# Kernel optimization log

Measured on AMD Instinct MI355X. Metric: run time of the kernel, lower is better.

Reference implementation:

```python
import math
import jax, jax.numpy as jnp
import numpy as np

# hyperparameters (module defaults; w_scale overridden to 1.0)
EMA_SPEED = 0.05
REW_SENS = 1.0
LR = 0.0033
MOMENTUM = 0.4
UNTANH = 0.6
SPEED = 0.5
WIDTH = 0.1
WD = 0.01
LAT_DECAY = 0.01
NOISE_SCALE = 0.8
C_MOMENT = 0.99
W_SCALE = 1.0


def rms_norm(x, axis=-1):
    return x * jax.lax.rsqrt(jnp.mean(x * x, axis=axis, keepdims=True) + 1e-6)


def setup_inputs() -> dict:
    key = jax.random.key(0)
    ks = jax.random.split(key, 16)
    B, N, D = 16, 128, 64
    s = 1.0 / math.sqrt(D)
    return {
        'eye_env': jax.random.normal(ks[0], (B, D), jnp.float32),
        'stomach_env': jax.random.normal(ks[1], (B, D), jnp.float32),
        'state': jax.random.normal(ks[2], (B, N, D), jnp.float32),
        'output': jax.random.normal(ks[3], (B, N, D), jnp.float32),
        'W1': jax.random.normal(ks[4], (B, N, D, D), jnp.float32) * s,
        'W2': jax.random.normal(ks[5], (B, N, D, D), jnp.float32) * s,
        'W3': jax.random.normal(ks[6], (B, N, D, D), jnp.float32) * s,
        'M1': jax.random.normal(ks[7], (B, N, D, D), jnp.float32) * 0.2,
        'M2': jax.random.normal(ks[8], (B, N, D, D), jnp.float32) * 0.2,
        'M3': jax.random.normal(ks[9], (B, N, D, D), jnp.float32) * 0.2,
        'E_baseline': jax.random.uniform(ks[10], (B, N, D), jnp.float32),
        'A': jax.nn.softmax(jax.random.normal(ks[11], (B, N, N), jnp.float32), axis=2),
        'noise_A': jax.random.normal(ks[12], (B, N, N), jnp.float32),
        'noise1_raw': jax.random.normal(ks[13], (B, N, D), jnp.float32),
        'noise2_raw': jax.random.normal(ks[14], (B, N, D), jnp.float32),
        'step_counter': 0,
    }


def reference(eye_env, stomach_env, state, output, W1, W2, W3, M1, M2, M3,
              E_baseline, A, noise_A, noise1_raw, noise2_raw, step_counter):
    B, N, D = state.shape
    sc = jnp.float32(step_counter) + 1.0  # self.step_counter += 1

    # attention routing
    q = jnp.einsum('bnj,bnjk->bnk', state, W3)
    k = jnp.einsum('bnj,bnjk->bnk', state, W2)
    raw_A = jnp.einsum('bnd,bmd->bnm', q, k) / math.sqrt(D) + noise_A * 1e-5
    P_dense = jax.nn.softmax(raw_A, axis=2)
    keep = (P_dense > 1.0 / (N + 1.0)) | (P_dense == jnp.max(P_dense, axis=2, keepdims=True))
    P = jax.nn.softmax(jnp.where(keep, raw_A, -jnp.inf), axis=2)
    A_new = A * C_MOMENT + P * (1.0 - C_MOMENT)
    A_new = A_new.at[:, 0:2, :].set(0.0)

    # message passing + sensory clamp
    target = jnp.einsum('bnm,bmd->bnd', A_new, output)
    target = target.at[:, 0].set(eye_env).at[:, 1].set(stomach_env)

    # prediction
    raw_pred = jnp.einsum('bnj,bnjk->bnk', state, W1)
    raw = raw_pred - jnp.tanh(raw_pred) * UNTANH
    prediction = jnp.tanh(raw) * math.sqrt(2.0 + math.sqrt(2.0))

    err = prediction - target
    E_curr = jax.nn.softmax(err, axis=-1)
    bmask = (E_baseline == 0).astype(jnp.float32)
    Eb = E_baseline * (1.0 - bmask) + E_curr * bmask
    Eb = Eb * (1.0 - EMA_SPEED) + EMA_SPEED * E_curr
    advantage = E_curr - Eb
    R = -rms_norm(advantage[..., None] * REW_SENS)  # (B,N,D,1)
    mask = (Eb > 0).astype(jnp.float32)[..., None]

    # noise injection
    state_mag = jnp.sum(jnp.abs(state), axis=(-2, -1), keepdims=True)
    noise1 = noise1_raw / (1.0 + state_mag)
    noise2 = noise2_raw * jnp.std(err, ddof=1) * NOISE_SCALE
    noisy_state = state + noise1 + noise2

    # Hebbian outer-product gradient, G_NORM=1.0 -> rms-normalized
    lg = -jnp.einsum('bni,bnj->bnij', err, noisy_state)
    lg = rms_norm(lg, axis=(2, 3))

    plasticity = 1.0 - R
    grad1 = plasticity * lg * mask + LAT_DECAY * W3 - WD * W1
    grad2 = plasticity * lg * mask + LAT_DECAY * W1 - WD * W2
    grad3 = plasticity * lg * mask + LAT_DECAY * W2 - WD * W3

    # travelling gaussian column mask
    idx = jnp.arange(D, dtype=jnp.float32).reshape(1, 1, 1, D)
    center = (sc * SPEED) % D
    diff = jnp.abs(idx - center)
    diff = jnp.minimum(diff, D - diff)
    g_mask = jnp.exp(-diff ** 2 / (2.0 * WIDTH ** 2 + 1e-6))

    M1n = M1 * MOMENTUM + (1.0 - MOMENTUM) * (grad1 * g_mask)
    M2n = M2 * MOMENTUM + (1.0 - MOMENTUM) * (grad2 * g_mask)
    M3n = M3 * MOMENTUM + (1.0 - MOMENTUM) * (grad3 * g_mask)
    W1n = rms_norm(W1 + LR * M1n) * W_SCALE
    W2n = rms_norm(W2 + LR * M2n) * W_SCALE
    W3n = rms_norm(W3 + LR * M3n) * W_SCALE

    # new output = prediction, new state = target
    return prediction, target, A_new, W1n, W2n, W3n
```

## Files before the change

### kernel.cpp

```cpp
#include <hip/hip_runtime.h>
#include <hip/hip_bf16.h>

typedef __hip_bfloat16 bf16;

__device__ __forceinline__ float b2f(bf16 x) { return __bfloat162float(x); }

template<bool F32>
__device__ __forceinline__ float ld(const void* p, size_t i) {
  if constexpr (F32) return ((const float*)p)[i];
  else return b2f(((const bf16*)p)[i]);
}

template<bool F32>
__device__ __forceinline__ void ld8(const void* p, size_t i, float v[8]) {
  if constexpr (F32) {
    const float4 a = *(const float4*)((const float*)p + i);
    const float4 b = *(const float4*)((const float*)p + i + 4);
    v[0]=a.x; v[1]=a.y; v[2]=a.z; v[3]=a.w;
    v[4]=b.x; v[5]=b.y; v[6]=b.z; v[7]=b.w;
  } else {
    union { uint4 u; bf16 h[8]; } t;
    t.u = *(const uint4*)((const bf16*)p + i);
    #pragma unroll
    for (int c = 0; c < 8; ++c) v[c] = b2f(t.h[c]);
  }
}


__global__ void k0_detect(const void* __restrict__ state, int* __restrict__ flag) {
  const int tid = threadIdx.x;
  bool huge = false;
  for (int i = tid; i < 1024; i += 64) {
    const float x = b2f(((const bf16*)state)[i]);
    if (!(fabsf(x) < 1e5f)) huge = true;
  }
  const unsigned long long m = __ballot(huge);
  if (tid == 0) *flag = (m != 0ull) ? 1 : 0;
}

template<bool F32>
__device__ __forceinline__ void k1_body(
    const void* state, const void* W1, const void* W2, const void* W3,
    float* qw, float* kw, float* pw, float* mag, float* out_pred,
    float* s_state, float (*s_part)[4][64])
{
  const int node = blockIdx.x;
  const int b = node >> 7;
  const int g = threadIdx.x >> 6;
  const int k = threadIdx.x & 63;
  if (threadIdx.x < 64) s_state[threadIdx.x] = ld<F32>(state, (size_t)node*64 + threadIdx.x);
  __syncthreads();
  const size_t nb = (size_t)node * 4096;
  float aq = 0.f, ak = 0.f, ap = 0.f;
  #pragma unroll 4
  for (int jj = 0; jj < 16; ++jj) {
    const int j = g*16 + jj;
    const float sj = s_state[j];
    const size_t off = nb + (size_t)j*64 + k;
    aq += sj * ld<F32>(W3, off);
    ak += sj * ld<F32>(W2, off);
    ap += sj * ld<F32>(W1, off);
  }
  s_part[0][g][k] = aq; s_part[1][g][k] = ak; s_part[2][g][k] = ap;
  __syncthreads();
  if (g == 0) {
    const float qv = s_part[0][0][k] + s_part[0][1][k] + s_part[0][2][k] + s_part[0][3][k];
    const float kv = s_part[1][0][k] + s_part[1][1][k] + s_part[1][2][k] + s_part[1][3][k];
    const float rp = s_part[2][0][k] + s_part[2][1][k] + s_part[2][2][k] + s_part[2][3][k];
    qw[(size_t)node*64 + k] = qv;
    kw[(size_t)node*64 + k] = kv;
    const float raw  = rp - tanhf(rp) * 0.6f;
    const float pred = tanhf(raw) * 1.8477590650225735f;
    pw[(size_t)node*64 + k] = pred;
    out_pred[(size_t)node*64 + k] = pred;
  } else if (g == 1) {
    float a = fabsf(s_state[k]);
    #pragma unroll
    for (int s = 32; s; s >>= 1) a += __shfl_xor(a, s, 64);
    if (k == 0) atomicAdd(&mag[b], a);
  }
}

__global__ __launch_bounds__(256) void k1_qkpred(
    const int* __restrict__ flag,
    const void* __restrict__ state,
    const void* __restrict__ W1, const void* __restrict__ W2,
    const void* __restrict__ W3,
    float* __restrict__ qw, float* __restrict__ kw, float* __restrict__ pw,
    float* __restrict__ mag, float* __restrict__ out_pred)
{
  __shared__ float s_state[64];
  __shared__ float s_part[3][4][64];
  if (*flag) k1_body<true >(state, W1, W2, W3, qw, kw, pw, mag, out_pred, s_state, s_part);
  else       k1_body<false>(state, W1, W2, W3, qw, kw, pw, mag, out_pred, s_state, s_part);
}

template<bool F32>
__device__ __forceinline__ void k2_body(
    const float* qw, const float* kw, const float* pw,
    const void* noiseA, const void* Aold, const void* outp_in,
    const void* eye, const void* stomach, const void* Ebase,
    float* errw, float* plw, float* stats,
    float* out_target, float* out_A,
    float* s_q, float* s_red, float* s_A)
{
  const int node = blockIdx.x;
  const int b = node >> 7, n = node & 127;
  const int m = threadIdx.x;
  if (m < 64) s_q[m] = qw[(size_t)node*64 + m];
  __syncthreads();
  const float4* k4 = (const float4*)(kw + ((size_t)(b*128 + m)) * 64);
  float dot = 0.f;
  #pragma unroll
  for (int i = 0; i < 16; ++i) {
    const float4 v = k4[i];
    dot += s_q[4*i]*v.x + s_q[4*i+1]*v.y + s_q[4*i+2]*v.z + s_q[4*i+3]*v.w;
  }
  const float raw = dot * 0.125f + 1e-5f * ld<F32>(noiseA, (size_t)node*128 + m);
  s_red[m] = raw; __syncthreads();
  for (int s = 64; s >= 1; s >>= 1) { if (m < s) s_red[m] = fmaxf(s_red[m], s_red[m+s]); __syncthreads(); }
  const float rmax = s_red[0]; __syncthreads();
  const float e = expf(raw - rmax);
  s_red[m] = e; __syncthreads();
  for (int s = 64; s >= 1; s >>= 1) { if (m < s) s_red[m] += s_red[m+s]; __syncthreads(); }
  const float S = s_red[0]; __syncthreads();
  const float Pd = e / S;
  const bool keep = (Pd > 0.007751937984496124f) || (raw == rmax);
  const float ek = keep ? e : 0.f;
  s_red[m] = ek; __syncthreads();
  for (int s = 64; s >= 1; s >>= 1) { if (m < s) s_red[m] += s_red[m+s]; __syncthreads(); }
  const float Sk = s_red[0];
  const float P = ek / Sk;
  const float An = (n < 2) ? 0.f
                 : 0.99f * ld<F32>(Aold, (size_t)node*128 + m) + 0.01f * P;
  s_A[m] = An;
  out_A[(size_t)node*128 + m] = An;
  __syncthreads();
  if (m < 64) {
    float t;
    if (n == 0)      t = ld<F32>(eye, b*64 + m);
    else if (n == 1) t = ld<F32>(stomach, b*64 + m);
    else {
      t = 0.f;
      for (int mm = 0; mm < 128; ++mm)
        t += s_A[mm] * ld<F32>(outp_in, ((size_t)b*128 + mm)*64 + m);
    }
    out_target[(size_t)node*64 + m] = t;
    const float er = pw[(size_t)node*64 + m] - t;
    errw[(size_t)node*64 + m] = er;
    float mx = er;
    #pragma unroll
    for (int s = 32; s; s >>= 1) mx = fmaxf(mx, __shfl_xor(mx, s, 64));
    const float ee = expf(er - mx);
    float ssum = ee;
    #pragma unroll
    for (int s = 32; s; s >>= 1) ssum += __shfl_xor(ssum, s, 64);
    const float Ec = ee / ssum;
    const float Ebl = ld<F32>(Ebase, (size_t)node*64 + m);
    const float Eb0 = (Ebl == 0.f) ? Ec : Ebl;
    const float Eb  = Eb0 * 0.95f + 0.05f * Ec;
    const float adv = Ec - Eb;
    const float R = -adv * rsqrtf(adv*adv + 1e-6f);
    const float maskv = (Eb > 0.f) ? 1.f : 0.f;
    plw[(size_t)node*64 + m] = (1.f - R) * maskv;
    float se = er, se2 = er*er;
    #pragma unroll
    for (int s = 32; s; s >>= 1) { se += __shfl_xor(se, s, 64); se2 += __shfl_xor(se2, s, 64); }
    if (m == 0) { atomicAdd(&stats[0], se); atomicAdd(&stats[1], se2); }
  }
}

__global__ __launch_bounds__(128) void k2_attn(
    const int* __restrict__ flag,
    const float* __restrict__ qw, const float* __restrict__ kw,
    const float* __restrict__ pw,
    const void* __restrict__ noiseA, const void* __restrict__ Aold,
    const void* __restrict__ outp_in,
    const void* __restrict__ eye, const void* __restrict__ stomach,
    const void* __restrict__ Ebase,
    float* __restrict__ errw, float* __restrict__ plw,
    float* __restrict__ stats,
    float* __restrict__ out_target, float* __restrict__ out_A)
{
  __shared__ float s_q[64];
  __shared__ float s_red[128];
  __shared__ float s_A[128];
  if (*flag) k2_body<true >(qw,kw,pw,noiseA,Aold,outp_in,eye,stomach,Ebase,errw,plw,stats,out_target,out_A,s_q,s_red,s_A);
  else       k2_body<false>(qw,kw,pw,noiseA,Aold,outp_in,eye,stomach,Ebase,errw,plw,stats,out_target,out_A,s_q,s_red,s_A);
}

template<bool F32>
__device__ __forceinline__ void k3_body(
    const float* errw, const float* plw,
    const void* state, const void* n1raw, const void* n2raw,
    const float* mag, const float* stats, const int* stepc,
    const void* W1, const void* W2, const void* W3,
    const void* M1, const void* M2, const void* M3,
    float* oW1, float* oW2, float* oW3,
    float* s_err, float* s_ns, float* s_pe, float* s_c, float* s_g)
{
  const int node = blockIdx.x;
  const int b = node >> 7;
  const int tid = threadIdx.x;
  if (tid < 64) {
    s_err[tid] = errw[(size_t)node*64 + tid];
  } else if (tid < 128) {
    const int i = tid - 64;
    const float S1 = stats[0], S2 = stats[1];
    const float Mn = 131072.f;
    const float var = (S2 - S1*S1/Mn) / (Mn - 1.f);
    const float stdv = sqrtf(fmaxf(var, 0.f));
    const float st = ld<F32>(state, (size_t)node*64 + i);
    s_ns[i] = st + ld<F32>(n1raw, (size_t)node*64 + i) / (1.f + mag[b])
                 + ld<F32>(n2raw, (size_t)node*64 + i) * stdv * 0.8f;
  }
  __syncthreads();
  if (tid < 64) {
    float e2 = s_err[tid]*s_err[tid];
    float n2 = s_ns[tid]*s_ns[tid];
    #pragma unroll
    for (int s = 32; s; s >>= 1) { e2 += __shfl_xor(e2, s, 64); n2 += __shfl_xor(n2, s, 64); }
    const float f = rsqrtf(e2 * n2 * (1.f/4096.f) + 1e-6f);
    s_c[tid] = -s_ns[tid] * f;
    const float sc = (float)stepc[0] + 1.f;
    const float center = fmodf(sc * 0.5f, 64.f);
    float diff = fabsf((float)tid - center);
    diff = fminf(diff, 64.f - diff);
    s_g[tid] = expf(-diff*diff * (1.f/0.020001f));
    s_pe[tid] = plw[(size_t)node*64 + tid] * s_err[tid];
  }
  __syncthreads();
  const size_t nb = (size_t)node * 4096;
  const int lane8 = tid & 7;
  #pragma unroll
  for (int pass = 0; pass < 2; ++pass) {
    const int r = (tid >> 3) + pass*32;
    const size_t off = nb + (size_t)r*64 + lane8*8;
    float w1v[8], w2v[8], w3v[8], m1v[8], m2v[8], m3v[8];
    ld8<F32>(W1, off, w1v); ld8<F32>(W2, off, w2v); ld8<F32>(W3, off, w3v);
    ld8<F32>(M1, off, m1v); ld8<F32>(M2, off, m2v); ld8<F32>(M3, off, m3v);
    const float pe = s_pe[r];
    float t1[8], t2[8], t3[8];
    float ss1 = 0.f, ss2 = 0.f, ss3 = 0.f;
    #pragma unroll
    for (int c = 0; c < 8; ++c) {
      const int j = lane8*8 + c;
      const float lgterm = pe * s_c[j];
      const float g = s_g[j];
      const float g1 = lgterm + 0.01f*w3v[c] - 0.01f*w1v[c];
      const float g2 = lgterm + 0.01f*w1v[c] - 0.01f*w2v[c];
      const float g3 = lgterm + 0.01f*w2v[c] - 0.01f*w3v[c];
      const float v1 = w1v[c] + 0.0033f*(0.4f*m1v[c] + 0.6f*g1*g);
      const float v2 = w2v[c] + 0.0033f*(0.4f*m2v[c] + 0.6f*g2*g);
      const float v3 = w3v[c] + 0.0033f*(0.4f*m3v[c] + 0.6f*g3*g);
      t1[c] = v1; t2[c] = v2; t3[c] = v3;
      ss1 += v1*v1; ss2 += v2*v2; ss3 += v3*v3;
    }
    #pragma unroll
    for (int s = 1; s <= 4; s <<= 1) {
      ss1 += __shfl_xor(ss1, s, 64);
      ss2 += __shfl_xor(ss2, s, 64);
      ss3 += __shfl_xor(ss3, s, 64);
    }
    const float r1 = rsqrtf(ss1*(1.f/64.f) + 1e-6f);
    const float r2 = rsqrtf(ss2*(1.f/64.f) + 1e-6f);
    const float r3 = rsqrtf(ss3*(1.f/64.f) + 1e-6f);
    float4 a, bb;
    a = make_float4(t1[0]*r1, t1[1]*r1, t1[2]*r1, t1[3]*r1);
    bb = make_float4(t1[4]*r1, t1[5]*r1, t1[6]*r1, t1[7]*r1);
    *(float4*)(oW1 + off) = a; *(float4*)(oW1 + off + 4) = bb;
    a = make_float4(t2[0]*r2, t2[1]*r2, t2[2]*r2, t2[3]*r2);
    bb = make_float4(t2[4]*r2, t2[5]*r2, t2[6]*r2, t2[7]*r2);
    *(float4*)(oW2 + off) = a; *(float4*)(oW2 + off + 4) = bb;
    a = make_float4(t3[0]*r3, t3[1]*r3, t3[2]*r3, t3[3]*r3);
    bb = make_float4(t3[4]*r3, t3[5]*r3, t3[6]*r3, t3[7]*r3);
    *(float4*)(oW3 + off) = a; *(float4*)(oW3 + off + 4) = bb;
  }
}

__global__ __launch_bounds__(256) void k3_update(
    const int* __restrict__ flag,
    const float* __restrict__ errw, const float* __restrict__ plw,
    const void* __restrict__ state, const void* __restrict__ n1raw,
    const void* __restrict__ n2raw,
    const float* __restrict__ mag, const float* __restrict__ stats,
    const int* __restrict__ stepc,
    const void* __restrict__ W1, const void* __restrict__ W2,
    const void* __restrict__ W3,
    const void* __restrict__ M1, const void* __restrict__ M2,
    const void* __restrict__ M3,
    float* __restrict__ oW1, float* __restrict__ oW2, float* __restrict__ oW3)
{
  __shared__ float s_err[64], s_ns[64], s_pe[64], s_c[64], s_g[64];
  if (*flag) k3_body<true >(errw,plw,state,n1raw,n2raw,mag,stats,stepc,W1,W2,W3,M1,M2,M3,oW1,oW2,oW3,s_err,s_ns,s_pe,s_c,s_g);
  else       k3_body<false>(errw,plw,state,n1raw,n2raw,mag,stats,stepc,W1,W2,W3,M1,M2,M3,oW1,oW2,oW3,s_err,s_ns,s_pe,s_c,s_g);
}

extern "C" void kernel_launch(void* const* d_in, const int* in_sizes, int n_in,
                              void* d_out, int out_size, void* d_ws, size_t ws_size,
                              hipStream_t stream) {
  const void* eye     = d_in[0];
  const void* stomach = d_in[1];
  const void* state   = d_in[2];
  const void* outp    = d_in[3];
  const void* W1      = d_in[4];
  const void* W2      = d_in[5];
  const void* W3      = d_in[6];
  const void* M1      = d_in[7];
  const void* M2      = d_in[8];
  const void* M3      = d_in[9];
  const void* Ebase   = d_in[10];
  const void* Aold    = d_in[11];
  const void* noiseA  = d_in[12];
  const void* n1raw   = d_in[13];
  const void* n2raw   = d_in[14];
  const int*  stepc   = (const int*)d_in[15];

  float* ws    = (float*)d_ws;
  float* qw    = ws;
  float* kw    = ws + 131072;
  float* pw    = ws + 262144;
  float* errw  = ws + 393216;
  float* plw   = ws + 524288;
  float* mag   = ws + 655360;
  float* stats = ws + 655376;
  int*   flag  = (int*)(ws + 655378);

  float* out        = (float*)d_out;
  float* out_pred   = out;
  float* out_target = out + 131072;
  float* out_A      = out + 262144;
  float* oW1        = out + 524288;
  float* oW2        = out + 8912896;
  float* oW3        = out + 17301504;

  hipMemsetAsync(mag, 0, 18 * sizeof(float), stream);
  k0_detect<<<1, 64, 0, stream>>>(state, flag);
  k1_qkpred<<<2048, 256, 0, stream>>>(flag, state, W1, W2, W3, qw, kw, pw, mag, out_pred);
  k2_attn<<<2048, 128, 0, stream>>>(flag, qw, kw, pw, noiseA, Aold, outp, eye, stomach,
                                    Ebase, errw, plw, stats, out_target, out_A);
  k3_update<<<2048, 256, 0, stream>>>(flag, errw, plw, state, n1raw, n2raw, mag, stats,
                                      stepc, W1, W2, W3, M1, M2, M3, oW1, oW2, oW3);
}
```

Baseline: 368.3 us.

## Restructure all three kernels: fold detect, tile attention, widen update blocks

Removes the separate dtype-detect launch by folding the detection into every k1 block. k1 now issues all weight loads up front and reduces partials with lane shuffles. k2 handles 8 query rows per block with K staged in shared memory, which cuts the grid from 2048 to 256 blocks. k3 runs 512 threads per node so each thread handles one row, issues its W/M loads before the first barrier, and uses nontemporal loads and stores for the streaming M inputs and W outputs. The pred workspace buffer is dropped in favour of reading out_pred. The costs are redundant detection reads in every k1 block, much larger shared memory in k2, and fewer k2 blocks for parallelism.

Measured after the change: 348.3 us. 1.06x faster.

```diff
diff --git a/kernel.cpp b/kernel.cpp
--- a/kernel.cpp
+++ b/kernel.cpp
@@ -2,6 +2,7 @@
 #include <hip/hip_bf16.h>
 
 typedef __hip_bfloat16 bf16;
+typedef float f32x4 __attribute__((ext_vector_type(4)));
 
 __device__ __forceinline__ float b2f(bf16 x) { return __bfloat162float(x); }
 
@@ -9,6 +10,19 @@
 __device__ __forceinline__ float ld(const void* p, size_t i) {
   if constexpr (F32) return ((const float*)p)[i];
   else return b2f(((const bf16*)p)[i]);
+}
+
+template<bool F32>
+__device__ __forceinline__ void ld4(const void* p, size_t i, float v[4]) {
+  if constexpr (F32) {
+    const float4 a = *(const float4*)((const float*)p + i);
+    v[0]=a.x; v[1]=a.y; v[2]=a.z; v[3]=a.w;
+  } else {
+    union { uint2 u; bf16 h[4]; } t;
+    t.u = *(const uint2*)((const bf16*)p + i);
+    #pragma unroll
+    for (int c = 0; c < 4; ++c) v[c] = b2f(t.h[c]);
+  }
 }
 
 template<bool F32>
@@ -26,167 +40,263 @@
   }
 }
 
-
-__global__ void k0_detect(const void* __restrict__ state, int* __restrict__ flag) {
-  const int tid = threadIdx.x;
-  bool huge = false;
-  for (int i = tid; i < 1024; i += 64) {
-    const float x = b2f(((const bf16*)state)[i]);
-    if (!(fabsf(x) < 1e5f)) huge = true;
-  }
-  const unsigned long long m = __ballot(huge);
-  if (tid == 0) *flag = (m != 0ull) ? 1 : 0;
-}
+template<bool F32>
+__device__ __forceinline__ void ld8nt(const void* p, size_t i, float v[8]) {
+  if constexpr (F32) {
+    const f32x4* q = (const f32x4*)((const float*)p + i);
+    const f32x4 a = __builtin_nontemporal_load(q);
+    const f32x4 b = __builtin_nontemporal_load(q + 1);
+    v[0]=a[0]; v[1]=a[1]; v[2]=a[2]; v[3]=a[3];
+    v[4]=b[0]; v[5]=b[1]; v[6]=b[2]; v[7]=b[3];
+  } else {
+    ld8<false>(p, i, v);
+  }
+}
+
+__device__ __forceinline__ float plast(float Ec, float Ebl) {
+  const float Eb0 = (Ebl == 0.f) ? Ec : Ebl;
+  const float Eb  = Eb0 * 0.95f + 0.05f * Ec;
+  const float adv = Ec - Eb;
+  const float R   = -adv * rsqrtf(adv*adv + 1e-6f);
+  return (Eb > 0.f) ? (1.f - R) : 0.f;
+}
+
 
 template<bool F32>
 __device__ __forceinline__ void k1_body(
     const void* state, const void* W1, const void* W2, const void* W3,
-    float* qw, float* kw, float* pw, float* mag, float* out_pred,
-    float* s_state, float (*s_part)[4][64])
+    float* qw, float* kw, float* mag, float* out_pred,
+    float* s_state, float* s_part)
 {
   const int node = blockIdx.x;
   const int b = node >> 7;
-  const int g = threadIdx.x >> 6;
-  const int k = threadIdx.x & 63;
-  if (threadIdx.x < 64) s_state[threadIdx.x] = ld<F32>(state, (size_t)node*64 + threadIdx.x);
-  __syncthreads();
+  const int tid = threadIdx.x;
+  const int w = tid >> 6, lane = tid & 63;
+  const int jg = lane >> 4, cq = lane & 15;
+  const int c0 = cq * 4;
   const size_t nb = (size_t)node * 4096;
-  float aq = 0.f, ak = 0.f, ap = 0.f;
-  #pragma unroll 4
-  for (int jj = 0; jj < 16; ++jj) {
-    const int j = g*16 + jj;
-    const float sj = s_state[j];
-    const size_t off = nb + (size_t)j*64 + k;
-    aq += sj * ld<F32>(W3, off);
-    ak += sj * ld<F32>(W2, off);
-    ap += sj * ld<F32>(W1, off);
-  }
-  s_part[0][g][k] = aq; s_part[1][g][k] = ak; s_part[2][g][k] = ap;
-  __syncthreads();
-  if (g == 0) {
-    const float qv = s_part[0][0][k] + s_part[0][1][k] + s_part[0][2][k] + s_part[0][3][k];
-    const float kv = s_part[1][0][k] + s_part[1][1][k] + s_part[1][2][k] + s_part[1][3][k];
-    const float rp = s_part[2][0][k] + s_part[2][1][k] + s_part[2][2][k] + s_part[2][3][k];
-    qw[(size_t)node*64 + k] = qv;
-    kw[(size_t)node*64 + k] = kv;
-    const float raw  = rp - tanhf(rp) * 0.6f;
-    const float pred = tanhf(raw) * 1.8477590650225735f;
-    pw[(size_t)node*64 + k] = pred;
-    out_pred[(size_t)node*64 + k] = pred;
-  } else if (g == 1) {
-    float a = fabsf(s_state[k]);
+
+  float w3v[4][4], w2v[4][4], w1v[4][4];
+  #pragma unroll
+  for (int jj = 0; jj < 4; ++jj) {
+    const int j = w*16 + jg*4 + jj;
+    const size_t o = nb + (size_t)j*64 + c0;
+    ld4<F32>(W3, o, w3v[jj]);
+    ld4<F32>(W2, o, w2v[jj]);
+    ld4<F32>(W1, o, w1v[jj]);
+  }
+  if (tid < 64) s_state[tid] = ld<F32>(state, (size_t)node*64 + tid);
+  __syncthreads();
+
+  float aq[4] = {0,0,0,0}, ak[4] = {0,0,0,0}, ap[4] = {0,0,0,0};
+  #pragma unroll
+  for (int jj = 0; jj < 4; ++jj) {
+    const float sj = s_state[w*16 + jg*4 + jj];
+    #pragma unroll
+    for (int cc = 0; cc < 4; ++cc) {
+      aq[cc] += sj * w3v[jj][cc];
+      ak[cc] += sj * w2v[jj][cc];
+      ap[cc] += sj * w1v[jj][cc];
+    }
+  }
+  #pragma unroll
+  for (int cc = 0; cc < 4; ++cc) {
+    aq[cc] += __shfl_xor(aq[cc], 16, 64); aq[cc] += __shfl_xor(aq[cc], 32, 64);
+    ak[cc] += __shfl_xor(ak[cc], 16, 64); ak[cc] += __shfl_xor(ak[cc], 32, 64);
+    ap[cc] += __shfl_xor(ap[cc], 16, 64); ap[cc] += __shfl_xor(ap[cc], 32, 64);
+  }
+  if (jg == 0) {
+    *(float4*)&s_part[w*192 +  0 + c0] = make_float4(aq[0], aq[1], aq[2], aq[3]);
+    *(float4*)&s_part[w*192 + 64 + c0] = make_float4(ak[0], ak[1], ak[2], ak[3]);
+    *(float4*)&s_part[w*192 +128 + c0] = make_float4(ap[0], ap[1], ap[2], ap[3]);
+  }
+  if (w == 3) {
+    float a = fabsf(s_state[lane]);
     #pragma unroll
     for (int s = 32; s; s >>= 1) a += __shfl_xor(a, s, 64);
-    if (k == 0) atomicAdd(&mag[b], a);
+    if (lane == 0) atomicAdd(&mag[b], a);
+  }
+  __syncthreads();
+  if (tid < 192) {
+    const int mat = tid >> 6, col = tid & 63;
+    const float v = s_part[0*192 + mat*64 + col] + s_part[1*192 + mat*64 + col]
+                  + s_part[2*192 + mat*64 + col] + s_part[3*192 + mat*64 + col];
+    if (mat == 0)      qw[(size_t)node*64 + col] = v;
+    else if (mat == 1) kw[(size_t)node*64 + col] = v;
+    else {
+      const float raw  = v - tanhf(v) * 0.6f;
+      out_pred[(size_t)node*64 + col] = tanhf(raw) * 1.8477590650225735f;
+    }
   }
 }
 
 __global__ __launch_bounds__(256) void k1_qkpred(
-    const int* __restrict__ flag,
     const void* __restrict__ state,
     const void* __restrict__ W1, const void* __restrict__ W2,
     const void* __restrict__ W3,
-    float* __restrict__ qw, float* __restrict__ kw, float* __restrict__ pw,
-    float* __restrict__ mag, float* __restrict__ out_pred)
-{
-  __shared__ float s_state[64];
-  __shared__ float s_part[3][4][64];
-  if (*flag) k1_body<true >(state, W1, W2, W3, qw, kw, pw, mag, out_pred, s_state, s_part);
-  else       k1_body<false>(state, W1, W2, W3, qw, kw, pw, mag, out_pred, s_state, s_part);
+    float* __restrict__ qw, float* __restrict__ kw,
+    float* __restrict__ mag, float* __restrict__ out_pred,
+    int* __restrict__ flagws)
+{
+  __shared__ alignas(16) float s_state[64];
+  __shared__ alignas(16) float s_part[768];
+  __shared__ int s_flag;
+  const int tid = threadIdx.x;
+  bool huge = false;
+  for (int i = tid; i < 1024; i += 256) {
+    const float x = b2f(((const bf16*)state)[i]);
+    if (!(fabsf(x) < 1e5f)) huge = true;
+  }
+  const unsigned long long m = __ballot(huge);
+  if (tid == 0) s_flag = 0;
+  __syncthreads();
+  if ((tid & 63) == 0 && m != 0ull) s_flag = 1;
+  __syncthreads();
+  const bool f32 = (s_flag != 0);
+  if (blockIdx.x == 0 && tid == 0) *flagws = f32 ? 1 : 0;
+  if (f32) k1_body<true >(state, W1, W2, W3, qw, kw, mag, out_pred, s_state, s_part);
+  else     k1_body<false>(state, W1, W2, W3, qw, kw, mag, out_pred, s_state, s_part);
 }
 
 template<bool F32>
 __device__ __forceinline__ void k2_body(
-    const float* qw, const float* kw, const float* pw,
-    const void* noiseA, const void* Aold, const void* outp_in,
+    const float* qw, const float* kw, const float* predw,
+    const void* noiseA, const void* Aold, const void* outp,
     const void* eye, const void* stomach, const void* Ebase,
     float* errw, float* plw, float* stats,
     float* out_target, float* out_A,
-    float* s_q, float* s_red, float* s_A)
-{
-  const int node = blockIdx.x;
-  const int b = node >> 7, n = node & 127;
-  const int m = threadIdx.x;
-  if (m < 64) s_q[m] = qw[(size_t)node*64 + m];
-  __syncthreads();
-  const float4* k4 = (const float4*)(kw + ((size_t)(b*128 + m)) * 64);
-  float dot = 0.f;
-  #pragma unroll
-  for (int i = 0; i < 16; ++i) {
-    const float4 v = k4[i];
-    dot += s_q[4*i]*v.x + s_q[4*i+1]*v.y + s_q[4*i+2]*v.z + s_q[4*i+3]*v.w;
-  }
-  const float raw = dot * 0.125f + 1e-5f * ld<F32>(noiseA, (size_t)node*128 + m);
-  s_red[m] = raw; __syncthreads();
-  for (int s = 64; s >= 1; s >>= 1) { if (m < s) s_red[m] = fmaxf(s_red[m], s_red[m+s]); __syncthreads(); }
-  const float rmax = s_red[0]; __syncthreads();
-  const float e = expf(raw - rmax);
-  s_red[m] = e; __syncthreads();
-  for (int s = 64; s >= 1; s >>= 1) { if (m < s) s_red[m] += s_red[m+s]; __syncthreads(); }
-  const float S = s_red[0]; __syncthreads();
-  const float Pd = e / S;
-  const bool keep = (Pd > 0.007751937984496124f) || (raw == rmax);
-  const float ek = keep ? e : 0.f;
-  s_red[m] = ek; __syncthreads();
-  for (int s = 64; s >= 1; s >>= 1) { if (m < s) s_red[m] += s_red[m+s]; __syncthreads(); }
-  const float Sk = s_red[0];
-  const float P = ek / Sk;
-  const float An = (n < 2) ? 0.f
-                 : 0.99f * ld<F32>(Aold, (size_t)node*128 + m) + 0.01f * P;
-  s_A[m] = An;
-  out_A[(size_t)node*128 + m] = An;
-  __syncthreads();
-  if (m < 64) {
-    float t;
-    if (n == 0)      t = ld<F32>(eye, b*64 + m);
-    else if (n == 1) t = ld<F32>(stomach, b*64 + m);
-    else {
-      t = 0.f;
-      for (int mm = 0; mm < 128; ++mm)
-        t += s_A[mm] * ld<F32>(outp_in, ((size_t)b*128 + mm)*64 + m);
-    }
-    out_target[(size_t)node*64 + m] = t;
-    const float er = pw[(size_t)node*64 + m] - t;
-    errw[(size_t)node*64 + m] = er;
-    float mx = er;
-    #pragma unroll
-    for (int s = 32; s; s >>= 1) mx = fmaxf(mx, __shfl_xor(mx, s, 64));
-    const float ee = expf(er - mx);
-    float ssum = ee;
-    #pragma unroll
-    for (int s = 32; s; s >>= 1) ssum += __shfl_xor(ssum, s, 64);
-    const float Ec = ee / ssum;
-    const float Ebl = ld<F32>(Ebase, (size_t)node*64 + m);
-    const float Eb0 = (Ebl == 0.f) ? Ec : Ebl;
-    const float Eb  = Eb0 * 0.95f + 0.05f * Ec;
-    const float adv = Ec - Eb;
-    const float R = -adv * rsqrtf(adv*adv + 1e-6f);
-    const float maskv = (Eb > 0.f) ? 1.f : 0.f;
-    plw[(size_t)node*64 + m] = (1.f - R) * maskv;
-    float se = er, se2 = er*er;
-    #pragma unroll
-    for (int s = 32; s; s >>= 1) { se += __shfl_xor(se, s, 64); se2 += __shfl_xor(se2, s, 64); }
-    if (m == 0) { atomicAdd(&stats[0], se); atomicAdd(&stats[1], se2); }
-  }
-}
-
-__global__ __launch_bounds__(128) void k2_attn(
+    float* s_k, float* s_q, float* s_A)
+{
+  const int bidx = blockIdx.x;
+  const int b = bidx >> 4;
+  const int n0 = (bidx & 15) * 8;
+  const int tid = threadIdx.x;
+
+  {
+    const float* kwb = kw + (size_t)b * 8192;
+    #pragma unroll
+    for (int it = 0; it < 8; ++it) {
+      const int idx = it*256 + tid;
+      const int m = idx >> 4, dq = idx & 15;
+      const float4 v = *(const float4*)(kwb + (size_t)idx * 4);
+      float* dst = &s_k[m*65 + dq*4];
+      dst[0] = v.x; dst[1] = v.y; dst[2] = v.z; dst[3] = v.w;
+    }
+    if (tid < 128) {
+      const int rr = tid >> 4, dq = tid & 15;
+      *(float4*)&s_q[rr*64 + dq*4] =
+          *(const float4*)(qw + ((size_t)(b*128 + n0 + rr))*64 + dq*4);
+    }
+  }
+  __syncthreads();
+
+  const int rr = tid >> 5, c = tid & 31;
+  const int n = n0 + rr;
+  const size_t node = (size_t)b*128 + n;
+
+  float acc[4] = {0.f, 0.f, 0.f, 0.f};
+  {
+    const float* qrow = s_q + rr*64;
+    #pragma unroll 8
+    for (int j = 0; j < 64; ++j) {
+      const float qv = qrow[j];
+      acc[0] += qv * s_k[(c     )*65 + j];
+      acc[1] += qv * s_k[(c + 32)*65 + j];
+      acc[2] += qv * s_k[(c + 64)*65 + j];
+      acc[3] += qv * s_k[(c + 96)*65 + j];
+    }
+  }
+  float raw[4];
+  #pragma unroll
+  for (int i = 0; i < 4; ++i)
+    raw[i] = acc[i]*0.125f + 1e-5f*ld<F32>(noiseA, node*128 + c + 32*i);
+
+  float rmx = fmaxf(fmaxf(raw[0], raw[1]), fmaxf(raw[2], raw[3]));
+  #pragma unroll
+  for (int s = 16; s >= 1; s >>= 1) rmx = fmaxf(rmx, __shfl_xor(rmx, s, 64));
+  float e[4], S = 0.f;
+  #pragma unroll
+  for (int i = 0; i < 4; ++i) { e[i] = expf(raw[i] - rmx); S += e[i]; }
+  #pragma unroll
+  for (int s = 16; s >= 1; s >>= 1) S += __shfl_xor(S, s, 64);
+  float ek[4], Sk = 0.f;
+  #pragma unroll
+  for (int i = 0; i < 4; ++i) {
+    const float Pd = e[i] / S;
+    ek[i] = ((Pd > 0.007751937984496124f) || (raw[i] == rmx)) ? e[i] : 0.f;
+    Sk += ek[i];
+  }
+  #pragma unroll
+  for (int s = 16; s >= 1; s >>= 1) Sk += __shfl_xor(Sk, s, 64);
+  #pragma unroll
+  for (int i = 0; i < 4; ++i) {
+    const int m = c + 32*i;
+    const float P = ek[i] / Sk;
+    const float An = (n < 2) ? 0.f
+                   : 0.99f * ld<F32>(Aold, node*128 + m) + 0.01f * P;
+    out_A[node*128 + m] = An;
+    s_A[rr*128 + m] = An;
+  }
+  __syncthreads();
+
+  float t0, t1;
+  if (n == 0) {
+    t0 = ld<F32>(eye, (size_t)b*64 + c);
+    t1 = ld<F32>(eye, (size_t)b*64 + c + 32);
+  } else if (n == 1) {
+    t0 = ld<F32>(stomach, (size_t)b*64 + c);
+    t1 = ld<F32>(stomach, (size_t)b*64 + c + 32);
+  } else {
+    t0 = 0.f; t1 = 0.f;
+    const float* arow = s_A + rr*128;
+    const size_t ob = (size_t)b * 8192;
+    #pragma unroll 4
+    for (int m = 0; m < 128; ++m) {
+      const float a = arow[m];
+      t0 += a * ld<F32>(outp, ob + m*64 + c);
+      t1 += a * ld<F32>(outp, ob + m*64 + c + 32);
+    }
+  }
+  out_target[node*64 + c]      = t0;
+  out_target[node*64 + c + 32] = t1;
+  const float e0 = predw[node*64 + c]      - t0;
+  const float e1 = predw[node*64 + c + 32] - t1;
+  errw[node*64 + c]      = e0;
+  errw[node*64 + c + 32] = e1;
+
+  float mx = fmaxf(e0, e1);
+  #pragma unroll
+  for (int s = 16; s >= 1; s >>= 1) mx = fmaxf(mx, __shfl_xor(mx, s, 64));
+  const float x0 = expf(e0 - mx), x1 = expf(e1 - mx);
+  float ss = x0 + x1;
+  #pragma unroll
+  for (int s = 16; s >= 1; s >>= 1) ss += __shfl_xor(ss, s, 64);
+  plw[node*64 + c]      = plast(x0/ss, ld<F32>(Ebase, node*64 + c));
+  plw[node*64 + c + 32] = plast(x1/ss, ld<F32>(Ebase, node*64 + c + 32));
+
+  float se = e0 + e1, sq = e0*e0 + e1*e1;
+  #pragma unroll
+  for (int s = 16; s >= 1; s >>= 1) { se += __shfl_xor(se, s, 64); sq += __shfl_xor(sq, s, 64); }
+  if (c == 0) { atomicAdd(&stats[0], se); atomicAdd(&stats[1], sq); }
+}
+
+__global__ __launch_bounds__(256) void k2_attn(
     const int* __restrict__ flag,
     const float* __restrict__ qw, const float* __restrict__ kw,
-    const float* __restrict__ pw,
+    const float* __restrict__ predw,
     const void* __restrict__ noiseA, const void* __restrict__ Aold,
-    const void* __restrict__ outp_in,
+    const void* __restrict__ outp,
     const void* __restrict__ eye, const void* __restrict__ stomach,
     const void* __restrict__ Ebase,
     float* __restrict__ errw, float* __restrict__ plw,
     float* __restrict__ stats,
     float* __restrict__ out_target, float* __restrict__ out_A)
 {
-  __shared__ float s_q[64];
-  __shared__ float s_red[128];
-  __shared__ float s_A[128];
-  if (*flag) k2_body<true >(qw,kw,pw,noiseA,Aold,outp_in,eye,stomach,Ebase,errw,plw,stats,out_target,out_A,s_q,s_red,s_A);
-  else       k2_body<false>(qw,kw,pw,noiseA,Aold,outp_in,eye,stomach,Ebase,errw,plw,stats,out_target,out_A,s_q,s_red,s_A);
+  __shared__ alignas(16) float s_k[128*65];
+  __shared__ alignas(16) float s_q[8*64];
+  __shared__ alignas(16) float s_A[8*128];
+  if (*flag) k2_body<true >(qw,kw,predw,noiseA,Aold,outp,eye,stomach,Ebase,errw,plw,stats,out_target,out_A,s_k,s_q,s_A);
+  else       k2_body<false>(qw,kw,predw,noiseA,Aold,outp,eye,stomach,Ebase,errw,plw,stats,out_target,out_A,s_k,s_q,s_A);
 }
 
 template<bool F32>
@@ -203,82 +313,86 @@
   const int b = node >> 7;
   const int tid = threadIdx.x;
   if (tid < 64) {
-    s_err[tid] = errw[(size_t)node*64 + tid];
+    const float e = errw[(size_t)node*64 + tid];
+    s_err[tid] = e;
+    s_pe[tid]  = plw[(size_t)node*64 + tid] * e;
   } else if (tid < 128) {
     const int i = tid - 64;
     const float S1 = stats[0], S2 = stats[1];
     const float Mn = 131072.f;
     const float var = (S2 - S1*S1/Mn) / (Mn - 1.f);
     const float stdv = sqrtf(fmaxf(var, 0.f));
-    const float st = ld<F32>(state, (size_t)node*64 + i);
-    s_ns[i] = st + ld<F32>(n1raw, (size_t)node*64 + i) / (1.f + mag[b])
-                 + ld<F32>(n2raw, (size_t)node*64 + i) * stdv * 0.8f;
-  }
-  __syncthreads();
+    s_ns[i] = ld<F32>(state, (size_t)node*64 + i)
+            + ld<F32>(n1raw, (size_t)node*64 + i) / (1.f + mag[b])
+            + ld<F32>(n2raw, (size_t)node*64 + i) * stdv * 0.8f;
+  } else if (tid < 192) {
+    const int i = tid - 128;
+    const float sc = (float)stepc[0] + 1.f;
+    const float center = fmodf(sc * 0.5f, 64.f);
+    float diff = fabsf((float)i - center);
+    diff = fminf(diff, 64.f - diff);
+    s_g[i] = expf(-diff*diff * (1.f/0.020001f));
+  }
+
+  const int r = tid >> 3;
+  const int l8 = tid & 7;
+  const size_t off = (size_t)node*4096 + (size_t)r*64 + (size_t)l8*8;
+  float w1v[8], w2v[8], w3v[8], m1v[8], m2v[8], m3v[8];
+  ld8  <F32>(W1, off, w1v); ld8  <F32>(W2, off, w2v); ld8  <F32>(W3, off, w3v);
+  ld8nt<F32>(M1, off, m1v); ld8nt<F32>(M2, off, m2v); ld8nt<F32>(M3, off, m3v);
+  __syncthreads();
+
   if (tid < 64) {
     float e2 = s_err[tid]*s_err[tid];
     float n2 = s_ns[tid]*s_ns[tid];
     #pragma unroll
     for (int s = 32; s; s >>= 1) { e2 += __shfl_xor(e2, s, 64); n2 += __shfl_xor(n2, s, 64); }
-    const float f = rsqrtf(e2 * n2 * (1.f/4096.f) + 1e-6f);
-    s_c[tid] = -s_ns[tid] * f;
-    const float sc = (float)stepc[0] + 1.f;
-    const float center = fmodf(sc * 0.5f, 64.f);
-    float diff = fabsf((float)tid - center);
-    diff = fminf(diff, 64.f - diff);
-    s_g[tid] = expf(-diff*diff * (1.f/0.020001f));
-    s_pe[tid] = plw[(size_t)node*64 + tid] * s_err[tid];
-  }
-  __syncthreads();
-  const size_t nb = (size_t)node * 4096;
-  const int lane8 = tid & 7;
-  #pragma unroll
-  for (int pass = 0; pass < 2; ++pass) {
-    const int r = (tid >> 3) + pass*32;
-    const size_t off = nb + (size_t)r*64 + lane8*8;
-    float w1v[8], w2v[8], w3v[8], m1v[8], m2v[8], m3v[8];
-    ld8<F32>(W1, off, w1v); ld8<F32>(W2, off, w2v); ld8<F32>(W3, off, w3v);
-    ld8<F32>(M1, off, m1v); ld8<F32>(M2, off, m2v); ld8<F32>(M3, off, m3v);
-    const float pe = s_pe[r];
-    float t1[8], t2[8], t3[8];
-    float ss1 = 0.f, ss2 = 0.f, ss3 = 0.f;
-    #pragma unroll
-    for (int c = 0; c < 8; ++c) {
-      const int j = lane8*8 + c;
-      const float lgterm = pe * s_c[j];
-      const float g = s_g[j];
-      const float g1 = lgterm + 0.01f*w3v[c] - 0.01f*w1v[c];
-      const float g2 = lgterm + 0.01f*w1v[c] - 0.01f*w2v[c];
-      const float g3 = lgterm + 0.01f*w2v[c] - 0.01f*w3v[c];
-      const float v1 = w1v[c] + 0.0033f*(0.4f*m1v[c] + 0.6f*g1*g);
-      const float v2 = w2v[c] + 0.0033f*(0.4f*m2v[c] + 0.6f*g2*g);
-      const float v3 = w3v[c] + 0.0033f*(0.4f*m3v[c] + 0.6f*g3*g);
-      t1[c] = v1; t2[c] = v2; t3[c] = v3;
-      ss1 += v1*v1; ss2 += v2*v2; ss3 += v3*v3;
-    }
-    #pragma unroll
-    for (int s = 1; s <= 4; s <<= 1) {
-      ss1 += __shfl_xor(ss1, s, 64);
-      ss2 += __shfl_xor(ss2, s, 64);
-      ss3 += __shfl_xor(ss3, s, 64);
-    }
-    const float r1 = rsqrtf(ss1*(1.f/64.f) + 1e-6f);
-    const float r2 = rsqrtf(ss2*(1.f/64.f) + 1e-6f);
-    const float r3 = rsqrtf(ss3*(1.f/64.f) + 1e-6f);
-    float4 a, bb;
-    a = make_float4(t1[0]*r1, t1[1]*r1, t1[2]*r1, t1[3]*r1);
-    bb = make_float4(t1[4]*r1, t1[5]*r1, t1[6]*r1, t1[7]*r1);
-    *(float4*)(oW1 + off) = a; *(float4*)(oW1 + off + 4) = bb;
-    a = make_float4(t2[0]*r2, t2[1]*r2, t2[2]*r2, t2[3]*r2);
-    bb = make_float4(t2[4]*r2, t2[5]*r2, t2[6]*r2, t2[7]*r2);
-    *(float4*)(oW2 + off) = a; *(float4*)(oW2 + off + 4) = bb;
-    a = make_float4(t3[0]*r3, t3[1]*r3, t3[2]*r3, t3[3]*r3);
-    bb = make_float4(t3[4]*r3, t3[5]*r3, t3[6]*r3, t3[7]*r3);
-    *(float4*)(oW3 + off) = a; *(float4*)(oW3 + off + 4) = bb;
-  }
-}
-
-__global__ __launch_bounds__(256) void k3_update(
+    s_c[tid] = -s_ns[tid] * rsqrtf(e2 * n2 * (1.f/4096.f) + 1e-6f);
+  }
+  __syncthreads();
+
+  const float pe = s_pe[r];
+  float t1[8], t2[8], t3[8];
+  float ss1 = 0.f, ss2 = 0.f, ss3 = 0.f;
+  #pragma unroll
+  for (int cc = 0; cc < 8; ++cc) {
+    const int j = l8*8 + cc;
+    const float lgterm = pe * s_c[j];
+    const float g = s_g[j];
+    const float g1 = lgterm + 0.01f*w3v[cc] - 0.01f*w1v[cc];
+    const float g2 = lgterm + 0.01f*w1v[cc] - 0.01f*w2v[cc];
+    const float g3 = lgterm + 0.01f*w2v[cc] - 0.01f*w3v[cc];
+    const float v1 = w1v[cc] + 0.0033f*(0.4f*m1v[cc] + 0.6f*g1*g);
+    const float v2 = w2v[cc] + 0.0033f*(0.4f*m2v[cc] + 0.6f*g2*g);
+    const float v3 = w3v[cc] + 0.0033f*(0.4f*m3v[cc] + 0.6f*g3*g);
+    t1[cc] = v1; t2[cc] = v2; t3[cc] = v3;
+    ss1 += v1*v1; ss2 += v2*v2; ss3 += v3*v3;
+  }
+  #pragma unroll
+  for (int s = 1; s <= 4; s <<= 1) {
+    ss1 += __shfl_xor(ss1, s, 64);
+    ss2 += __shfl_xor(ss2, s, 64);
+    ss3 += __shfl_xor(ss3, s, 64);
+  }
+  const float r1 = rsqrtf(ss1*(1.f/64.f) + 1e-6f);
+  const float r2 = rsqrtf(ss2*(1.f/64.f) + 1e-6f);
+  const float r3 = rsqrtf(ss3*(1.f/64.f) + 1e-6f);
+  f32x4 o;
+  o[0]=t1[0]*r1; o[1]=t1[1]*r1; o[2]=t1[2]*r1; o[3]=t1[3]*r1;
+  __builtin_nontemporal_store(o, (f32x4*)(oW1 + off));
+  o[0]=t1[4]*r1; o[1]=t1[5]*r1; o[2]=t1[6]*r1; o[3]=t1[7]*r1;
+  __builtin_nontemporal_store(o, (f32x4*)(oW1 + off + 4));
+  o[0]=t2[0]*r2; o[1]=t2[1]*r2; o[2]=t2[2]*r2; o[3]=t2[3]*r2;
+  __builtin_nontemporal_store(o, (f32x4*)(oW2 + off));
+  o[0]=t2[4]*r2; o[1]=t2[5]*r2; o[2]=t2[6]*r2; o[3]=t2[7]*r2;
+  __builtin_nontemporal_store(o, (f32x4*)(oW2 + off + 4));
+  o[0]=t3[0]*r3; o[1]=t3[1]*r3; o[2]=t3[2]*r3; o[3]=t3[3]*r3;
+  __builtin_nontemporal_store(o, (f32x4*)(oW3 + off));
+  o[0]=t3[4]*r3; o[1]=t3[5]*r3; o[2]=t3[6]*r3; o[3]=t3[7]*r3;
+  __builtin_nontemporal_store(o, (f32x4*)(oW3 + off + 4));
+}
+
+__global__ __launch_bounds__(512, 2) void k3_update(
     const int* __restrict__ flag,
     const float* __restrict__ errw, const float* __restrict__ plw,
     const void* __restrict__ state, const void* __restrict__ n1raw,
@@ -291,7 +405,7 @@
     const void* __restrict__ M3,
     float* __restrict__ oW1, float* __restrict__ oW2, float* __restrict__ oW3)
 {
-  __shared__ float s_err[64], s_ns[64], s_pe[64], s_c[64], s_g[64];
+  __shared__ alignas(16) float s_err[64], s_ns[64], s_pe[64], s_c[64], s_g[64];
   if (*flag) k3_body<true >(errw,plw,state,n1raw,n2raw,mag,stats,stepc,W1,W2,W3,M1,M2,M3,oW1,oW2,oW3,s_err,s_ns,s_pe,s_c,s_g);
   else       k3_body<false>(errw,plw,state,n1raw,n2raw,mag,stats,stepc,W1,W2,W3,M1,M2,M3,oW1,oW2,oW3,s_err,s_ns,s_pe,s_c,s_g);
 }
@@ -319,12 +433,11 @@
   float* ws    = (float*)d_ws;
   float* qw    = ws;
   float* kw    = ws + 131072;
-  float* pw    = ws + 262144;
-  float* errw  = ws + 393216;
-  float* plw   = ws + 524288;
-  float* mag   = ws + 655360;
-  float* stats = ws + 655376;
-  int*   flag  = (int*)(ws + 655378);
+  float* errw  = ws + 262144;
+  float* plw   = ws + 393216;
+  float* mag   = ws + 524288;
+  float* stats = ws + 524304;
+  int*   flag  = (int*)(ws + 524306);
 
   float* out        = (float*)d_out;
   float* out_pred   = out;
@@ -335,10 +448,10 @@
   float* oW3        = out + 17301504;
 
   hipMemsetAsync(mag, 0, 18 * sizeof(float), stream);
-  k0_detect<<<1, 64, 0, stream>>>(state, flag);
-  k1_qkpred<<<2048, 256, 0, stream>>>(flag, state, W1, W2, W3, qw, kw, pw, mag, out_pred);
-  k2_attn<<<2048, 128, 0, stream>>>(flag, qw, kw, pw, noiseA, Aold, outp, eye, stomach,
-                                    Ebase, errw, plw, stats, out_target, out_A);
-  k3_update<<<2048, 256, 0, stream>>>(flag, errw, plw, state, n1raw, n2raw, mag, stats,
+  k1_qkpred<<<2048, 256, 0, stream>>>(state, W1, W2, W3, qw, kw, mag, out_pred, flag);
+  k2_attn<<<256, 256, 0, stream>>>(flag, qw, kw, out_pred, noiseA, Aold, outp,
+                                   eye, stomach, Ebase, errw, plw, stats,
+                                   out_target, out_A);
+  k3_update<<<2048, 512, 0, stream>>>(flag, errw, plw, state, n1raw, n2raw, mag, stats,
                                       stepc, W1, W2, W3, M1, M2, M3, oW1, oW2, oW3);
 }
```
